# Kernel optimization log

Measured on AMD Instinct MI355X. Metric: run time of the kernel, lower is better.

## Reference

```python
import math
import jax, jax.numpy as jnp
import numpy as np

EMBED_DIM = 128
NUM_HEADS = 2
B, N = 4096, 32  # batch of fully-connected ally graphs, N allies each (self-edges included)


def sparsemax(z, axis):
    """Sparsemax (Martins & Astudillo 2016) along `axis`."""
    K = z.shape[axis]
    z_sorted = -jnp.sort(-z, axis=axis)  # descending
    z_cumsum = jnp.cumsum(z_sorted, axis=axis)
    shape = [1] * z.ndim
    shape[axis] = K
    k = jnp.arange(1, K + 1, dtype=z.dtype).reshape(shape)
    support = (1.0 + k * z_sorted) > z_cumsum
    k_sup = jnp.sum(support.astype(z.dtype), axis=axis, keepdims=True)
    tau = (jnp.sum(jnp.where(support, z_sorted, 0.0), axis=axis, keepdims=True) - 1.0) / k_sup
    return jnp.maximum(z - tau, 0.0)


def setup_inputs() -> dict:
    key = jax.random.key(0)
    k1, k2, k3, k4 = jax.random.split(key, 4)
    D, H = EMBED_DIM, NUM_HEADS
    node_feature = jax.random.normal(k1, (B, N, D), dtype=jnp.float32)
    scale = 1.0 / math.sqrt(D)
    WK = jax.random.normal(k2, (D, H * D), dtype=jnp.float32) * scale
    WV = jax.random.normal(k3, (D, H * D), dtype=jnp.float32) * scale
    WQ = jax.random.normal(k4, (D, H * D), dtype=jnp.float32) * scale
    return {"node_feature": node_feature, "WK": WK, "WV": WV, "WQ": WQ}


def reference(node_feature, WK, WV, WQ):
    D, H = EMBED_DIM, NUM_HEADS
    x = node_feature  # [B, N, D]
    # per-node projections; Linear(D, H*D) reshaped to (H, D) as in torch .view
    k = (x @ WK).reshape(B, N, H, D)
    v = (x @ WV).reshape(B, N, H, D)
    q = (x @ WQ).reshape(B, N, H, D)
    # fully connected graph: node i attends over mailbox of all nodes j in same graph
    score = jnp.einsum("bihd,bjhd->bijh", q, k) / math.sqrt(D * H)  # [B, N(i), N(j), H]
    w = sparsemax(score, axis=2)  # sparsemax over neighbor (mailbox) dim
    out = jnp.einsum("bijh,bjhd->bihd", w, v)  # weighted reduction
    out = out.mean(axis=2)  # mean over heads -> [B, N, D]
    output = out.reshape(B * N, D)
    # weight padded to max_num_allies (= N here, so no extra padding needed)
    weight = w.reshape(B * N, N, H)
    return output, weight
```

## Files before the change

kernel.cpp:

```cpp
#include <hip/hip_runtime.h>
#include <hip/hip_bf16.h>


#define NG 4096

typedef short bf16x8 __attribute__((ext_vector_type(8)));
typedef float f32x4 __attribute__((ext_vector_type(4)));

__device__ inline short f2bf(float f) {
    __hip_bfloat16 h = __float2bfloat16(f);
    return __builtin_bit_cast(short, h);
}
__device__ inline unsigned pack2(float a, float b) {
    return (unsigned)(unsigned short)f2bf(a) | ((unsigned)(unsigned short)f2bf(b) << 16);
}

#define TSWZ(node, col) ((((node) << 8)) + (((col) ^ (((node) & 7) << 3))))
#define VSWZ(row, col) ((((row) << 5) + (col)) ^ (((row) & 3) << 3))

__global__ void pack_mv_kernel(const float* __restrict__ WQ, const float* __restrict__ WK,
                               const float* __restrict__ WV,
                               short* __restrict__ pm, short* __restrict__ pv) {
    int gidx = blockIdx.x * 256 + threadIdx.x;
    if (gidx < 32768) {
        int idx  = gidx;
        int jj   = idx & 7;
        int lane = (idx >> 3) & 63;
        int s    = (idx >> 9) & 3;
        int mt   = (idx >> 11) & 15;
        int h    = mt >> 3;
        int a    = s * 32 + (lane >> 4) * 8 + jj;
        int bl   = (mt & 7) * 16 + (lane & 15);
        const float4* qa = (const float4*)(WQ + a * 256 + h * 128);
        const float4* kb = (const float4*)(WK + bl * 256 + h * 128);
        float acc = 0.f;
        #pragma unroll 8
        for (int c = 0; c < 32; ++c) {
            float4 q4 = qa[c], k4 = kb[c];
            acc += q4.x * k4.x + q4.y * k4.y + q4.z * k4.z + q4.w * k4.w;
        }
        pm[idx] = f2bf(acc * 0.0625f);
    } else {
        int idx  = gidx - 32768;
        int jj   = idx & 7;
        int lane = (idx >> 3) & 63;
        int s    = (idx >> 9) & 3;
        int t    = (idx >> 11) & 15;
        int krow = s * 32 + (lane >> 4) * 8 + jj;
        int col  = t * 16 + (lane & 15);
        pv[idx] = f2bf(WV[krow * 256 + col]);
    }
}

__global__ __launch_bounds__(256, 5)
void fused_attn_kernel(const float* __restrict__ x, const short* __restrict__ pm,
                       const short* __restrict__ pv, float* __restrict__ out,
                       float* __restrict__ wgt) {
    __shared__ char __align__(16) smem[32768];
    short* t_s  = (short*)smem;
    float* s_s  = (float*)smem;
    short* vT_s = (short*)(smem + 16384);

    int b    = blockIdx.x;
    int tid  = threadIdx.x;
    int lane = tid & 63;
    int wave = tid >> 6;
    int lrow = lane & 15;
    int quad = lane >> 4;

    bf16x8 xf[2][4];
    const float* xg = x + (size_t)b * 4096;
    #pragma unroll
    for (int nt = 0; nt < 2; ++nt)
        #pragma unroll
        for (int s = 0; s < 4; ++s) {
            const float* p0 = &xg[(nt * 16 + lrow) * 128 + s * 32 + quad * 8];
            float4 f0 = *(const float4*)p0;
            float4 f1 = *(const float4*)(p0 + 4);
            bf16x8 v;
            v[0]=f2bf(f0.x); v[1]=f2bf(f0.y); v[2]=f2bf(f0.z); v[3]=f2bf(f0.w);
            v[4]=f2bf(f1.x); v[5]=f2bf(f1.y); v[6]=f2bf(f1.z); v[7]=f2bf(f1.w);
            xf[nt][s] = v;
        }

    #pragma unroll
    for (int t = 0; t < 4; ++t) {
        int mt = wave * 4 + t;
        const short* pb = pm + (mt * 4) * 512 + lane * 8;
        bf16x8 wf[4];
        #pragma unroll
        for (int s = 0; s < 4; ++s) wf[s] = *(const bf16x8*)&pb[s * 512];
        f32x4 acc[2] = {{0.f,0.f,0.f,0.f},{0.f,0.f,0.f,0.f}};
        #pragma unroll
        for (int nt = 0; nt < 2; ++nt)
            #pragma unroll
            for (int s = 0; s < 4; ++s)
                acc[nt] = __builtin_amdgcn_mfma_f32_16x16x32_bf16(wf[s], xf[nt][s], acc[nt], 0, 0, 0);
        #pragma unroll
        for (int nt = 0; nt < 2; ++nt) {
            int node = nt * 16 + lrow;
            int addr = TSWZ(node, mt * 16 + quad * 4);
            uint2 pk; pk.x = pack2(acc[nt][0], acc[nt][1]); pk.y = pack2(acc[nt][2], acc[nt][3]);
            *(uint2*)&t_s[addr] = pk;
        }
    }
    #pragma unroll
    for (int t = 0; t < 4; ++t) {
        int ntv = wave * 4 + t;
        const short* pb = pv + (ntv * 4) * 512 + lane * 8;
        bf16x8 wf[4];
        #pragma unroll
        for (int s = 0; s < 4; ++s) wf[s] = *(const bf16x8*)&pb[s * 512];
        f32x4 acc[2] = {{0.f,0.f,0.f,0.f},{0.f,0.f,0.f,0.f}};
        #pragma unroll
        for (int mt = 0; mt < 2; ++mt)
            #pragma unroll
            for (int s = 0; s < 4; ++s)
                acc[mt] = __builtin_amdgcn_mfma_f32_16x16x32_bf16(xf[mt][s], wf[s], acc[mt], 0, 0, 0);
        #pragma unroll
        for (int mt = 0; mt < 2; ++mt) {
            int row = ntv * 16 + lrow;
            int idx = VSWZ(row, mt * 16 + quad * 4);
            uint2 pk; pk.x = pack2(acc[mt][0], acc[mt][1]); pk.y = pack2(acc[mt][2], acc[mt][3]);
            *(uint2*)&vT_s[idx] = pk;
        }
    }
    __syncthreads();

    f32x4 sacc[2];
    #pragma unroll
    for (int tt = 0; tt < 2; ++tt) {
        int ti = wave * 2 + tt;
        int h = ti >> 2, it = (ti >> 1) & 1, jt = ti & 1;
        f32x4 acc = {0.f, 0.f, 0.f, 0.f};
        #pragma unroll
        for (int s = 0; s < 4; ++s) {
            int node = it * 16 + lrow;
            bf16x8 at = *(const bf16x8*)&t_s[TSWZ(node, h * 128 + s * 32 + quad * 8)];
            acc = __builtin_amdgcn_mfma_f32_16x16x32_bf16(at, xf[jt][s], acc, 0, 0, 0);
        }
        sacc[tt] = acc;
    }
    __syncthreads();

    #pragma unroll
    for (int tt = 0; tt < 2; ++tt) {
        int ti = wave * 2 + tt;
        int h = ti >> 2, it = (ti >> 1) & 1, jt = ti & 1;
        #pragma unroll
        for (int r = 0; r < 4; ++r)
            s_s[(h * 32 + it * 16 + quad * 4 + r) * 36 + jt * 16 + lrow] = sacc[tt][r];
    }
    __syncthreads();

    {
        int j  = lane & 31;
        int hh = lane >> 5;
        #pragma unroll
        for (int ii = 0; ii < 8; ++ii) {
            int i   = wave * 8 + ii;
            int row = hh * 32 + i;
            const float* zr = &s_s[row * 36];
            float z[32];
            #pragma unroll
            for (int c = 0; c < 8; ++c) {
                float4 f = *(const float4*)&zr[c * 4];
                z[c*4] = f.x; z[c*4+1] = f.y; z[c*4+2] = f.z; z[c*4+3] = f.w;
            }
            float zj = zr[j];
            float c0 = 0.f, c1 = 0.f, s0 = 0.f, s1 = 0.f;
            #pragma unroll
            for (int l = 0; l < 32; l += 2) {
                float m0 = (z[l]     > zj) ? 1.f : 0.f;
                float m1 = (z[l + 1] > zj) ? 1.f : 0.f;
                c0 += m0;  s0 = __builtin_fmaf(m0, z[l],     s0);
                c1 += m1;  s1 = __builtin_fmaf(m1, z[l + 1], s1);
            }
            float rk  = c0 + c1 + 1.f;
            float cum = s0 + s1 + zj;
            float tc  = (cum - 1.f) / rk;
            #pragma unroll
            for (int m = 1; m <= 16; m <<= 1) tc = fmaxf(tc, __shfl_xor(tc, m, 32));
            float w = fmaxf(zj - tc, 0.f);
            ((short*)zr)[j] = f2bf(w);
            float wo = __shfl_xor(w, 32);
            if (lane < 32) {
                float2 v; v.x = w; v.y = wo;
                *(float2*)&wgt[((size_t)b * 32 + i) * 64 + j * 2] = v;
            }
        }
    }
    __syncthreads();

    #pragma unroll
    for (int tt = 0; tt < 4; ++tt) {
        int ti = wave * 4 + tt;
        int it = ti >> 3, dt = ti & 7;
        f32x4 acc = {0.f, 0.f, 0.f, 0.f};
        #pragma unroll
        for (int h = 0; h < 2; ++h) {
            int vrow = h * 128 + dt * 16 + lrow;
            bf16x8 aw = *(const bf16x8*)((short*)&s_s[(h * 32 + it * 16 + lrow) * 36] + quad * 8);
            bf16x8 bv = *(const bf16x8*)&vT_s[VSWZ(vrow, quad * 8)];
            acc = __builtin_amdgcn_mfma_f32_16x16x32_bf16(aw, bv, acc, 0, 0, 0);
        }
        #pragma unroll
        for (int r = 0; r < 4; ++r)
            out[((size_t)b * 32 + it * 16 + quad * 4 + r) * 128 + dt * 16 + lrow] = acc[r] * 0.5f;
    }
}

extern "C" void kernel_launch(void* const* d_in, const int* in_sizes, int n_in,
                              void* d_out, int out_size, void* d_ws, size_t ws_size,
                              hipStream_t stream) {
    const float* x  = (const float*)d_in[0];
    const float* WK = (const float*)d_in[1];
    const float* WV = (const float*)d_in[2];
    const float* WQ = (const float*)d_in[3];
    float* out = (float*)d_out;
    float* wgt = out + (size_t)NG * 32 * 128;
    short* pm = (short*)d_ws;
    short* pv = pm + 32768;

    hipLaunchKernelGGL(pack_mv_kernel, dim3(256), dim3(256), 0, stream, WQ, WK, WV, pm, pv);
    hipLaunchKernelGGL(fused_attn_kernel, dim3(NG), dim3(256), 0, stream, x, pm, pv, out, wgt);
}
```

Before: 202.7 us.

## Stage x through LDS with coalesced loads, reorganize score tiles, and defer weight stores

Node features are now loaded with fully coalesced float4 reads, converted to bf16 and staged in swizzled LDS, then read back into MFMA fragments, replacing strided per-lane global loads. The score-tile assignment is changed so each wave owns one head/row-tile and runs the sparsemax on its own rows, which removes one block barrier. Attention weights are no longer written as bf16-rounded values during sparsemax; they are read back from LDS after the PV matmul and stored as wider float4 writes. Occupancy hint drops from 5 to 4 blocks, and two extra barriers are added for the LDS staging. The stored weights are now bf16-rounded rather than fp32, which adds precision risk.

```diff
diff --git a/kernel.cpp b/kernel.cpp
--- a/kernel.cpp
+++ b/kernel.cpp
@@ -5,18 +5,23 @@
 #define NG 4096
 
 typedef short bf16x8 __attribute__((ext_vector_type(8)));
+typedef short bf16x4 __attribute__((ext_vector_type(4)));
 typedef float f32x4 __attribute__((ext_vector_type(4)));
 
 __device__ inline short f2bf(float f) {
     __hip_bfloat16 h = __float2bfloat16(f);
     return __builtin_bit_cast(short, h);
 }
+__device__ inline float bf2f(short s) {
+    return __builtin_bit_cast(float, ((unsigned)(unsigned short)s) << 16);
+}
 __device__ inline unsigned pack2(float a, float b) {
     return (unsigned)(unsigned short)f2bf(a) | ((unsigned)(unsigned short)f2bf(b) << 16);
 }
 
 #define TSWZ(node, col) ((((node) << 8)) + (((col) ^ (((node) & 7) << 3))))
 #define VSWZ(row, col) ((((row) << 5) + (col)) ^ (((row) & 3) << 3))
+#define XSWZ(node, col) (((node) << 7) + (((col) ^ (((node) & 7) << 3))))
 
 __global__ void pack_mv_kernel(const float* __restrict__ WQ, const float* __restrict__ WK,
                                const float* __restrict__ WV,
@@ -52,11 +57,12 @@
     }
 }
 
-__global__ __launch_bounds__(256, 5)
+__global__ __launch_bounds__(256, 4)
 void fused_attn_kernel(const float* __restrict__ x, const short* __restrict__ pm,
                        const short* __restrict__ pv, float* __restrict__ out,
                        float* __restrict__ wgt) {
     __shared__ char __align__(16) smem[32768];
+    short* x_l  = (short*)smem;
     short* t_s  = (short*)smem;
     float* s_s  = (float*)smem;
     short* vT_s = (short*)(smem + 16384);
@@ -68,20 +74,25 @@
     int lrow = lane & 15;
     int quad = lane >> 4;
 
+    const float* xg = x + (size_t)b * 4096;
+    #pragma unroll
+    for (int i = 0; i < 4; ++i) {
+        int flat4 = i * 256 + tid;
+        int node  = flat4 >> 5;
+        int c4    = (flat4 & 31) * 4;
+        float4 f  = *(const float4*)&xg[flat4 * 4];
+        uint2 pk; pk.x = pack2(f.x, f.y); pk.y = pack2(f.z, f.w);
+        *(uint2*)&x_l[XSWZ(node, c4)] = pk;
+    }
+    __syncthreads();
+
     bf16x8 xf[2][4];
-    const float* xg = x + (size_t)b * 4096;
     #pragma unroll
     for (int nt = 0; nt < 2; ++nt)
         #pragma unroll
-        for (int s = 0; s < 4; ++s) {
-            const float* p0 = &xg[(nt * 16 + lrow) * 128 + s * 32 + quad * 8];
-            float4 f0 = *(const float4*)p0;
-            float4 f1 = *(const float4*)(p0 + 4);
-            bf16x8 v;
-            v[0]=f2bf(f0.x); v[1]=f2bf(f0.y); v[2]=f2bf(f0.z); v[3]=f2bf(f0.w);
-            v[4]=f2bf(f1.x); v[5]=f2bf(f1.y); v[6]=f2bf(f1.z); v[7]=f2bf(f1.w);
-            xf[nt][s] = v;
-        }
+        for (int s = 0; s < 4; ++s)
+            xf[nt][s] = *(const bf16x8*)&x_l[XSWZ(nt * 16 + lrow, s * 32 + quad * 8)];
+    __syncthreads();
 
     #pragma unroll
     for (int t = 0; t < 4; ++t) {
@@ -129,9 +140,8 @@
 
     f32x4 sacc[2];
     #pragma unroll
-    for (int tt = 0; tt < 2; ++tt) {
-        int ti = wave * 2 + tt;
-        int h = ti >> 2, it = (ti >> 1) & 1, jt = ti & 1;
+    for (int jt = 0; jt < 2; ++jt) {
+        int h = wave >> 1, it = wave & 1;
         f32x4 acc = {0.f, 0.f, 0.f, 0.f};
         #pragma unroll
         for (int s = 0; s < 4; ++s) {
@@ -139,27 +149,22 @@
             bf16x8 at = *(const bf16x8*)&t_s[TSWZ(node, h * 128 + s * 32 + quad * 8)];
             acc = __builtin_amdgcn_mfma_f32_16x16x32_bf16(at, xf[jt][s], acc, 0, 0, 0);
         }
-        sacc[tt] = acc;
-    }
-    __syncthreads();
-
-    #pragma unroll
-    for (int tt = 0; tt < 2; ++tt) {
-        int ti = wave * 2 + tt;
-        int h = ti >> 2, it = (ti >> 1) & 1, jt = ti & 1;
+        sacc[jt] = acc;
+    }
+    __syncthreads();
+
+    #pragma unroll
+    for (int jt = 0; jt < 2; ++jt)
         #pragma unroll
         for (int r = 0; r < 4; ++r)
-            s_s[(h * 32 + it * 16 + quad * 4 + r) * 36 + jt * 16 + lrow] = sacc[tt][r];
-    }
-    __syncthreads();
+            s_s[(wave * 16 + quad * 4 + r) * 36 + jt * 16 + lrow] = sacc[jt][r];
 
     {
         int j  = lane & 31;
         int hh = lane >> 5;
         #pragma unroll
         for (int ii = 0; ii < 8; ++ii) {
-            int i   = wave * 8 + ii;
-            int row = hh * 32 + i;
+            int row = wave * 16 + hh * 8 + ii;
             const float* zr = &s_s[row * 36];
             float z[32];
             #pragma unroll
@@ -183,11 +188,6 @@
             for (int m = 1; m <= 16; m <<= 1) tc = fmaxf(tc, __shfl_xor(tc, m, 32));
             float w = fmaxf(zj - tc, 0.f);
             ((short*)zr)[j] = f2bf(w);
-            float wo = __shfl_xor(w, 32);
-            if (lane < 32) {
-                float2 v; v.x = w; v.y = wo;
-                *(float2*)&wgt[((size_t)b * 32 + i) * 64 + j * 2] = v;
-            }
         }
     }
     __syncthreads();
@@ -207,6 +207,18 @@
         #pragma unroll
         for (int r = 0; r < 4; ++r)
             out[((size_t)b * 32 + it * 16 + quad * 4 + r) * 128 + dt * 16 + lrow] = acc[r] * 0.5f;
+    }
+    {
+        int i  = tid >> 3;
+        int j2 = (tid & 7) * 4;
+        bf16x4 a0 = *(const bf16x4*)((short*)&s_s[i * 36] + j2);
+        bf16x4 a1 = *(const bf16x4*)((short*)&s_s[(32 + i) * 36] + j2);
+        float4 o0, o1;
+        o0.x = bf2f(a0[0]); o0.y = bf2f(a1[0]); o0.z = bf2f(a0[1]); o0.w = bf2f(a1[1]);
+        o1.x = bf2f(a0[2]); o1.y = bf2f(a1[2]); o1.z = bf2f(a0[3]); o1.w = bf2f(a1[3]);
+        float* wp = &wgt[((size_t)b * 32 + i) * 64 + j2 * 2];
+        *(float4*)wp = o0;
+        *(float4*)(wp + 4) = o1;
     }
 }
 
```

After: 185.7 us. -8.4%, faster.
